# Performance work log

Measured on AMD Instinct MI355X. Metric: run time of the kernel, lower is better.

The kernel has to match this reference:

```python
import jax, jax.numpy as jnp
import numpy as np

S, B, E, H = 2048, 2, 1024, 16
HD = E // H

def setup_inputs() -> dict:
    key = jax.random.key(0)
    ks = jax.random.split(key, 5)
    return {
        "query": jax.random.normal(ks[0], (S, B, E), dtype=jnp.float32),
        "key": jax.random.normal(ks[1], (S, B, E), dtype=jnp.float32),
        "value": jax.random.normal(ks[2], (S, B, E), dtype=jnp.float32),
        "in_proj_weight": jax.random.normal(ks[3], (3 * E, E), dtype=jnp.float32) * (E ** -0.5),
        "out_weight": jax.random.normal(ks[4], (E, E), dtype=jnp.float32) * (E ** -0.5),
    }

def reference(query, key, value, in_proj_weight, out_weight):
    # query: [S, B, E]; key/value are ignored by the original self-attn module.
    seq_len, bsz, embed_dim = query.shape
    head_dim = embed_dim // H
    scaling = head_dim ** -0.5
    # qkv projection: [S, B, 3E]; the torch view splits 3E as (H, 3, head_dim)
    qkv = jnp.einsum('sbe,fe->sbf', query, in_proj_weight)
    qkv = qkv.reshape(seq_len, bsz, H, 3, head_dim)
    q = qkv[..., 0, :]  # [S, B, H, hd]
    k = qkv[..., 1, :]
    v = qkv[..., 2, :]
    # scores: [B, H, S, S] (materialized, as in the unfused original)
    scores = jnp.einsum('sbhd,tbhd->bhst', q, k) * scaling
    probs = jax.nn.softmax(scores, axis=-1)
    attn = jnp.einsum('bhst,tbhd->sbhd', probs, v)
    attn = attn.reshape(seq_len, bsz, embed_dim)
    out = jnp.einsum('sbe,fe->sbf', attn, out_weight)
    return out
```

## Files before the change

### kernel.cpp

```cpp
#include <hip/hip_runtime.h>

typedef __attribute__((ext_vector_type(8))) short bf16x8;
typedef __attribute__((ext_vector_type(4))) float f32x4;
typedef __attribute__((ext_vector_type(8))) unsigned short u16x8;
typedef __attribute__((ext_vector_type(4))) unsigned short u16x4;

#define S_LEN 2048
#define BATCH 2
#define EMB 1024
#define NH 16
#define HDIM 64
#define M_ROWS (S_LEN * BATCH)
#define N_QKV (3 * EMB)

typedef const __attribute__((address_space(1))) unsigned int* gptr_t;
typedef __attribute__((address_space(3))) unsigned int* lptr_t;

__device__ __forceinline__ unsigned short f2b(float f) {
  union { float f; unsigned u; } v; v.f = f;
  unsigned r = v.u + 0x7fff + ((v.u >> 16) & 1);
  return (unsigned short)(r >> 16);
}
__device__ __forceinline__ unsigned short f2b_fast(float f) {
  union { float f; unsigned u; } v; v.f = f;
  return (unsigned short)((v.u + 0x8000u) >> 16);
}
__device__ __forceinline__ float b2f(unsigned short s) {
  union { float f; unsigned u; } v; v.u = ((unsigned)s) << 16;
  return v.f;
}

__global__ __launch_bounds__(256) void cvt_f32_bf16(const float* __restrict__ in,
                                                    unsigned short* __restrict__ out,
                                                    int n4) {
  int i = blockIdx.x * 256 + threadIdx.x;
  if (i >= n4) return;
  float4 a = reinterpret_cast<const float4*>(in)[i];
  u16x4 o;
  o[0] = f2b(a.x); o[1] = f2b(a.y); o[2] = f2b(a.z); o[3] = f2b(a.w);
  reinterpret_cast<u16x4*>(out)[i] = o;
}

template <int OUT_BF16>
__global__ __launch_bounds__(256) void gemm_bt(const unsigned short* __restrict__ A,
                                               const unsigned short* __restrict__ Bm,
                                               void* __restrict__ Cv,
                                               int Md, int Nd, int Kd) {
  __shared__ unsigned short As[128][32];
  __shared__ unsigned short Bs[128][32];
  int t = threadIdx.x;
  int bm = blockIdx.y, bn = blockIdx.x;
  int wid = t >> 6, lane = t & 63;
  int wr = wid >> 1, wc = wid & 1;
  int fr = lane & 15, fq = lane >> 4;
  int lrow = lane >> 2;
  int lcol = (lane & 3) * 8;

  f32x4 acc[4][4];
#pragma unroll
  for (int i = 0; i < 4; ++i)
#pragma unroll
    for (int j = 0; j < 4; ++j) acc[i][j] = (f32x4){0.f, 0.f, 0.f, 0.f};

  int nkt = Kd >> 5;
  for (int kt = 0; kt < nkt; ++kt) {
    const unsigned short* ga = A + (size_t)(bm * 128 + wid * 32 + lrow) * Kd + kt * 32 + lcol;
    const unsigned short* gb = Bm + (size_t)(bn * 128 + wid * 32 + lrow) * Kd + kt * 32 + lcol;
#pragma unroll
    for (int j = 0; j < 2; ++j) {
      __builtin_amdgcn_global_load_lds((gptr_t)(ga + (size_t)j * 16 * Kd),
                                       (lptr_t)&As[wid * 32 + j * 16][0], 16, 0, 0);
      __builtin_amdgcn_global_load_lds((gptr_t)(gb + (size_t)j * 16 * Kd),
                                       (lptr_t)&Bs[wid * 32 + j * 16][0], 16, 0, 0);
    }
    __syncthreads();

    bf16x8 af[4], bfv[4];
#pragma unroll
    for (int mt = 0; mt < 4; ++mt)
      af[mt] = *reinterpret_cast<const bf16x8*>(&As[wr * 64 + mt * 16 + fr][fq * 8]);
#pragma unroll
    for (int nt = 0; nt < 4; ++nt)
      bfv[nt] = *reinterpret_cast<const bf16x8*>(&Bs[wc * 64 + nt * 16 + fr][fq * 8]);
#pragma unroll
    for (int mt = 0; mt < 4; ++mt)
#pragma unroll
      for (int nt = 0; nt < 4; ++nt)
        acc[mt][nt] = __builtin_amdgcn_mfma_f32_16x16x32_bf16(af[mt], bfv[nt], acc[mt][nt], 0, 0, 0);
    __syncthreads();
  }

#pragma unroll
  for (int mt = 0; mt < 4; ++mt)
#pragma unroll
    for (int nt = 0; nt < 4; ++nt)
#pragma unroll
      for (int r = 0; r < 4; ++r) {
        int row = bm * 128 + wr * 64 + mt * 16 + fq * 4 + r;
        int col = bn * 128 + wc * 64 + nt * 16 + fr;
        float val = acc[mt][nt][r];
        if (OUT_BF16)
          reinterpret_cast<unsigned short*>(Cv)[(size_t)row * Nd + col] = f2b(val);
        else
          reinterpret_cast<float*>(Cv)[(size_t)row * Nd + col] = val;
      }
}

__global__ __launch_bounds__(256) void vtrans(const unsigned short* __restrict__ qkv,
                                              unsigned short* __restrict__ vt) {
  __shared__ unsigned short Ts[64][72];
  int t = threadIdx.x;
  int kb = blockIdx.x;
  int bh = blockIdx.y;
  int b = bh >> 4, h = bh & 15;
  int k0 = kb * 64;
#pragma unroll
  for (int i = 0; i < 2; ++i) {
    int c = t + i * 256;
    int r = c >> 3, q = c & 7;
    int chunk = q ^ ((r >> 3) & 7);
    *reinterpret_cast<u16x8*>(&Ts[r][chunk * 8]) =
        *reinterpret_cast<const u16x8*>(
            qkv + ((size_t)(k0 + r) * BATCH + b) * N_QKV + h * 192 + 128 + q * 8);
  }
  __syncthreads();
#pragma unroll
  for (int i = 0; i < 2; ++i) {
    int c = t + i * 256;
    int d = c >> 3, q = c & 7;
    u16x8 o;
#pragma unroll
    for (int j = 0; j < 8; ++j) {
      int k = q * 8 + j;
      int chunk = (d >> 3) ^ q;
      o[j] = Ts[k][chunk * 8 + (d & 7)];
    }
    *reinterpret_cast<u16x8*>(&vt[((size_t)bh * 64 + d) * S_LEN + k0 + q * 8]) = o;
  }
}

__global__ __launch_bounds__(256) void attn_kernel(const unsigned short* __restrict__ qkv,
                                                   const unsigned short* __restrict__ vt,
                                                   unsigned short* __restrict__ att) {
  __shared__ unsigned short Ks[2][64][72];
  __shared__ unsigned short VtS[2][64][72];
  __shared__ unsigned short Ps[4][16][72];
  int t = threadIdx.x;
  int wid = t >> 6, lane = t & 63;
  int fr = lane & 15, fq = lane >> 4;
  int bh = blockIdx.y;
  int b = bh >> 4;
  int h = bh & 15;
  int q0 = blockIdx.x * 64;

  int srow = t >> 3, sc8 = (t & 7) * 8;

  int qi = q0 + wid * 16 + fr;
  const unsigned short* qrow = qkv + ((size_t)qi * BATCH + b) * N_QKV + h * 192;
  bf16x8 qf[2];
  qf[0] = *reinterpret_cast<const bf16x8*>(qrow + fq * 8);
  qf[1] = *reinterpret_cast<const bf16x8*>(qrow + 32 + fq * 8);
#pragma unroll
  for (int c = 0; c < 2; ++c)
#pragma unroll
    for (int j = 0; j < 8; ++j)
      qf[c][j] = (short)f2b_fast(0.125f * b2f((unsigned short)qf[c][j]));

  f32x4 o[4];
#pragma unroll
  for (int dt = 0; dt < 4; ++dt) o[dt] = (f32x4){0.f, 0.f, 0.f, 0.f};
  float m_run[4], l_run[4];
#pragma unroll
  for (int r = 0; r < 4; ++r) { m_run[r] = -1e30f; l_run[r] = 0.f; }

#pragma unroll
  for (int i = 0; i < 2; ++i) {
    int row = srow + i * 32;
    *reinterpret_cast<u16x8*>(&Ks[0][row][sc8]) = *reinterpret_cast<const u16x8*>(
        qkv + ((size_t)row * BATCH + b) * N_QKV + h * 192 + 64 + sc8);
    *reinterpret_cast<u16x8*>(&VtS[0][row][sc8]) = *reinterpret_cast<const u16x8*>(
        vt + ((size_t)bh * 64 + row) * S_LEN + sc8);
  }
  __syncthreads();

  for (int kt = 0; kt < S_LEN / 64; ++kt) {
    int cur = kt & 1, nxt = cur ^ 1;

    u16x8 kreg[2], vreg[2];
    if (kt + 1 < S_LEN / 64) {
#pragma unroll
      for (int i = 0; i < 2; ++i) {
        int row = srow + i * 32;
        kreg[i] = *reinterpret_cast<const u16x8*>(
            qkv + ((size_t)((kt + 1) * 64 + row) * BATCH + b) * N_QKV + h * 192 + 64 + sc8);
        vreg[i] = *reinterpret_cast<const u16x8*>(
            vt + ((size_t)bh * 64 + row) * S_LEN + (kt + 1) * 64 + sc8);
      }
    }

    f32x4 sf[4];
#pragma unroll
    for (int nt = 0; nt < 4; ++nt) {
      bf16x8 bk0 = *reinterpret_cast<const bf16x8*>(&Ks[cur][nt * 16 + fr][fq * 8]);
      bf16x8 bk1 = *reinterpret_cast<const bf16x8*>(&Ks[cur][nt * 16 + fr][32 + fq * 8]);
      f32x4 s = (f32x4){0.f, 0.f, 0.f, 0.f};
      s = __builtin_amdgcn_mfma_f32_16x16x32_bf16(qf[0], bk0, s, 0, 0, 0);
      s = __builtin_amdgcn_mfma_f32_16x16x32_bf16(qf[1], bk1, s, 0, 0, 0);
      sf[nt] = s;
    }

    float p[4][4];
#pragma unroll
    for (int r = 0; r < 4; ++r) {
      float mx = fmaxf(fmaxf(sf[0][r], sf[1][r]), fmaxf(sf[2][r], sf[3][r]));
#pragma unroll
      for (int m = 1; m < 16; m <<= 1) mx = fmaxf(mx, __shfl_xor(mx, m));
      float mnew = fmaxf(m_run[r], mx);
      float alpha = __expf(m_run[r] - mnew);
      m_run[r] = mnew;
      float rs = 0.f;
#pragma unroll
      for (int nt = 0; nt < 4; ++nt) {
        float pv = __expf(sf[nt][r] - mnew);
        p[nt][r] = pv;
        rs += pv;
      }
#pragma unroll
      for (int m = 1; m < 16; m <<= 1) rs += __shfl_xor(rs, m);
      l_run[r] = l_run[r] * alpha + rs;
#pragma unroll
      for (int dt = 0; dt < 4; ++dt) o[dt][r] *= alpha;
    }

#pragma unroll
    for (int nt = 0; nt < 4; ++nt)
#pragma unroll
      for (int r = 0; r < 4; ++r)
        Ps[wid][fq * 4 + r][nt * 16 + fr] = f2b_fast(p[nt][r]);

#pragma unroll
    for (int kc = 0; kc < 2; ++kc) {
      bf16x8 pa = *reinterpret_cast<const bf16x8*>(&Ps[wid][fr][kc * 32 + fq * 8]);
#pragma unroll
      for (int dt = 0; dt < 4; ++dt) {
        bf16x8 vb = *reinterpret_cast<const bf16x8*>(&VtS[cur][dt * 16 + fr][kc * 32 + fq * 8]);
        o[dt] = __builtin_amdgcn_mfma_f32_16x16x32_bf16(pa, vb, o[dt], 0, 0, 0);
      }
    }

    if (kt + 1 < S_LEN / 64) {
#pragma unroll
      for (int i = 0; i < 2; ++i) {
        int row = srow + i * 32;
        *reinterpret_cast<u16x8*>(&Ks[nxt][row][sc8]) = kreg[i];
        *reinterpret_cast<u16x8*>(&VtS[nxt][row][sc8]) = vreg[i];
      }
    }
    __syncthreads();
  }

#pragma unroll
  for (int dt = 0; dt < 4; ++dt)
#pragma unroll
    for (int r = 0; r < 4; ++r) {
      int q = q0 + wid * 16 + fq * 4 + r;
      int d = dt * 16 + fr;
      float val = o[dt][r] / l_run[r];
      att[((size_t)q * BATCH + b) * EMB + h * 64 + d] = f2b(val);
    }
}

extern "C" void kernel_launch(void* const* d_in, const int* in_sizes, int n_in,
                              void* d_out, int out_size, void* d_ws, size_t ws_size,
                              hipStream_t stream) {
  const float* q_in  = (const float*)d_in[0];
  const float* w_in  = (const float*)d_in[3];
  const float* w_out = (const float*)d_in[4];
  float* out = (float*)d_out;

  unsigned short* ws  = (unsigned short*)d_ws;
  unsigned short* Xb  = ws;
  unsigned short* Wb  = Xb + (size_t)M_ROWS * EMB;
  unsigned short* Ob  = Wb + (size_t)N_QKV * EMB;
  unsigned short* QKV = Ob + (size_t)EMB * EMB;
  unsigned short* ATT = QKV + (size_t)M_ROWS * N_QKV;
  unsigned short* Vt  = Xb;

  cvt_f32_bf16<<<(M_ROWS * EMB / 4 + 255) / 256, 256, 0, stream>>>(q_in, Xb, M_ROWS * EMB / 4);
  cvt_f32_bf16<<<(N_QKV * EMB / 4 + 255) / 256, 256, 0, stream>>>(w_in, Wb, N_QKV * EMB / 4);
  cvt_f32_bf16<<<(EMB * EMB / 4 + 255) / 256, 256, 0, stream>>>(w_out, Ob, EMB * EMB / 4);

  gemm_bt<1><<<dim3(N_QKV / 128, M_ROWS / 128), 256, 0, stream>>>(Xb, Wb, QKV, M_ROWS, N_QKV, EMB);
  vtrans<<<dim3(S_LEN / 64, BATCH * NH), 256, 0, stream>>>(QKV, Vt);
  attn_kernel<<<dim3(S_LEN / 64, BATCH * NH), 256, 0, stream>>>(QKV, Vt, ATT);
  gemm_bt<0><<<dim3(EMB / 128, M_ROWS / 128), 256, 0, stream>>>(ATT, Ob, out, M_ROWS, EMB, EMB);
}
```

Measured before the change: 294.9 us.

## Transpose attention MFMA operands to keep P in registers and drop LDS staging

Swaps the A/B operands of the QK^T and PV MFMAs so each lane holds scores for a single query row. The row max and sum then need only two cross-lane shuffles instead of four per row, and the softmax state collapses to one scalar per lane. The P tile is regathered into MFMA operand layout with register shuffles rather than a round trip through shared memory, which removes the Ps buffer. The output is written as 4-wide vector stores, at the cost of extra shuffle and select instructions per tile.

```diff
diff --git a/kernel.cpp b/kernel.cpp
--- a/kernel.cpp
+++ b/kernel.cpp
@@ -144,7 +144,6 @@
                                                    unsigned short* __restrict__ att) {
   __shared__ unsigned short Ks[2][64][72];
   __shared__ unsigned short VtS[2][64][72];
-  __shared__ unsigned short Ps[4][16][72];
   int t = threadIdx.x;
   int wid = t >> 6, lane = t & 63;
   int fr = lane & 15, fq = lane >> 4;
@@ -169,9 +168,11 @@
   f32x4 o[4];
 #pragma unroll
   for (int dt = 0; dt < 4; ++dt) o[dt] = (f32x4){0.f, 0.f, 0.f, 0.f};
-  float m_run[4], l_run[4];
-#pragma unroll
-  for (int r = 0; r < 4; ++r) { m_run[r] = -1e30f; l_run[r] = 0.f; }
+  float m_run = -1e30f, l_run = 0.f;
+
+  int srcA = fr + ((fq & 1) << 5);
+  int srcB = srcA + 16;
+  int hi = (fq >> 1) & 1;
 
 #pragma unroll
   for (int i = 0; i < 2; ++i) {
@@ -198,53 +199,69 @@
       }
     }
 
-    f32x4 sf[4];
+    f32x4 snt[4];
 #pragma unroll
     for (int nt = 0; nt < 4; ++nt) {
       bf16x8 bk0 = *reinterpret_cast<const bf16x8*>(&Ks[cur][nt * 16 + fr][fq * 8]);
       bf16x8 bk1 = *reinterpret_cast<const bf16x8*>(&Ks[cur][nt * 16 + fr][32 + fq * 8]);
       f32x4 s = (f32x4){0.f, 0.f, 0.f, 0.f};
-      s = __builtin_amdgcn_mfma_f32_16x16x32_bf16(qf[0], bk0, s, 0, 0, 0);
-      s = __builtin_amdgcn_mfma_f32_16x16x32_bf16(qf[1], bk1, s, 0, 0, 0);
-      sf[nt] = s;
-    }
-
-    float p[4][4];
-#pragma unroll
-    for (int r = 0; r < 4; ++r) {
-      float mx = fmaxf(fmaxf(sf[0][r], sf[1][r]), fmaxf(sf[2][r], sf[3][r]));
-#pragma unroll
-      for (int m = 1; m < 16; m <<= 1) mx = fmaxf(mx, __shfl_xor(mx, m));
-      float mnew = fmaxf(m_run[r], mx);
-      float alpha = __expf(m_run[r] - mnew);
-      m_run[r] = mnew;
-      float rs = 0.f;
-#pragma unroll
-      for (int nt = 0; nt < 4; ++nt) {
-        float pv = __expf(sf[nt][r] - mnew);
-        p[nt][r] = pv;
+      s = __builtin_amdgcn_mfma_f32_16x16x32_bf16(bk0, qf[0], s, 0, 0, 0);
+      s = __builtin_amdgcn_mfma_f32_16x16x32_bf16(bk1, qf[1], s, 0, 0, 0);
+      snt[nt] = s;
+    }
+
+    float mx = fmaxf(fmaxf(fmaxf(snt[0][0], snt[0][1]), fmaxf(snt[0][2], snt[0][3])),
+                     fmaxf(fmaxf(snt[1][0], snt[1][1]), fmaxf(snt[1][2], snt[1][3])));
+    mx = fmaxf(mx, fmaxf(fmaxf(fmaxf(snt[2][0], snt[2][1]), fmaxf(snt[2][2], snt[2][3])),
+                         fmaxf(fmaxf(snt[3][0], snt[3][1]), fmaxf(snt[3][2], snt[3][3]))));
+    mx = fmaxf(mx, __shfl_xor(mx, 16));
+    mx = fmaxf(mx, __shfl_xor(mx, 32));
+    float mnew = fmaxf(m_run, mx);
+    float alpha = __expf(m_run - mnew);
+    m_run = mnew;
+    float rs = 0.f;
+#pragma unroll
+    for (int nt = 0; nt < 4; ++nt)
+#pragma unroll
+      for (int r = 0; r < 4; ++r) {
+        float pv = __expf(snt[nt][r] - mnew);
+        snt[nt][r] = pv;
         rs += pv;
       }
-#pragma unroll
-      for (int m = 1; m < 16; m <<= 1) rs += __shfl_xor(rs, m);
-      l_run[r] = l_run[r] * alpha + rs;
-#pragma unroll
-      for (int dt = 0; dt < 4; ++dt) o[dt][r] *= alpha;
-    }
-
+    rs += __shfl_xor(rs, 16);
+    rs += __shfl_xor(rs, 32);
+    l_run = l_run * alpha + rs;
+#pragma unroll
+    for (int dt = 0; dt < 4; ++dt) o[dt] *= alpha;
+
+    unsigned pd[8];
 #pragma unroll
     for (int nt = 0; nt < 4; ++nt)
 #pragma unroll
-      for (int r = 0; r < 4; ++r)
-        Ps[wid][fq * 4 + r][nt * 16 + fr] = f2b_fast(p[nt][r]);
+      for (int hh = 0; hh < 2; ++hh)
+        pd[nt * 2 + hh] = (unsigned)f2b_fast(snt[nt][2 * hh]) |
+                          ((unsigned)f2b_fast(snt[nt][2 * hh + 1]) << 16);
 
 #pragma unroll
     for (int kc = 0; kc < 2; ++kc) {
-      bf16x8 pa = *reinterpret_cast<const bf16x8*>(&Ps[wid][fr][kc * 32 + fq * 8]);
+      int base = kc * 4;
+      unsigned a0 = (unsigned)__shfl((int)pd[base + 0], srcA);
+      unsigned a1 = (unsigned)__shfl((int)pd[base + 1], srcA);
+      unsigned a2 = (unsigned)__shfl((int)pd[base + 2], srcA);
+      unsigned a3 = (unsigned)__shfl((int)pd[base + 3], srcA);
+      unsigned c0 = (unsigned)__shfl((int)pd[base + 0], srcB);
+      unsigned c1 = (unsigned)__shfl((int)pd[base + 1], srcB);
+      unsigned c2 = (unsigned)__shfl((int)pd[base + 2], srcB);
+      unsigned c3 = (unsigned)__shfl((int)pd[base + 3], srcB);
+      union { unsigned u[4]; bf16x8 v; } pb;
+      pb.u[0] = hi ? a2 : a0;
+      pb.u[1] = hi ? a3 : a1;
+      pb.u[2] = hi ? c2 : c0;
+      pb.u[3] = hi ? c3 : c1;
 #pragma unroll
       for (int dt = 0; dt < 4; ++dt) {
         bf16x8 vb = *reinterpret_cast<const bf16x8*>(&VtS[cur][dt * 16 + fr][kc * 32 + fq * 8]);
-        o[dt] = __builtin_amdgcn_mfma_f32_16x16x32_bf16(pa, vb, o[dt], 0, 0, 0);
+        o[dt] = __builtin_amdgcn_mfma_f32_16x16x32_bf16(vb, pb.v, o[dt], 0, 0, 0);
       }
     }
 
@@ -259,15 +276,16 @@
     __syncthreads();
   }
 
-#pragma unroll
-  for (int dt = 0; dt < 4; ++dt)
-#pragma unroll
-    for (int r = 0; r < 4; ++r) {
-      int q = q0 + wid * 16 + fq * 4 + r;
-      int d = dt * 16 + fr;
-      float val = o[dt][r] / l_run[r];
-      att[((size_t)q * BATCH + b) * EMB + h * 64 + d] = f2b(val);
-    }
+  float invl = 1.0f / l_run;
+  int q = q0 + wid * 16 + fr;
+#pragma unroll
+  for (int dt = 0; dt < 4; ++dt) {
+    u16x4 ov;
+#pragma unroll
+    for (int r = 0; r < 4; ++r) ov[r] = f2b(o[dt][r] * invl);
+    int d = dt * 16 + fq * 4;
+    *reinterpret_cast<u16x4*>(&att[((size_t)q * BATCH + b) * EMB + h * 64 + d]) = ov;
+  }
 }
 
 extern "C" void kernel_launch(void* const* d_in, const int* in_sizes, int n_in,
```

Measured after the change: 253.7 us. -14.0%, faster.

## Restructure attention to 128-query blocks with transposed MFMA and lazy rescale

Applied to the files above, without the earlier changes.

The attention kernel now handles two 16-query tiles per wave (128 queries per block), so each K/V tile loaded into LDS is reused twice. It computes S^T via swapped MFMA operands so each lane owns a query column, which reduces the softmax reductions to two cross-lane shuffles. P is passed to the PV MFMA through register shuffles instead of an LDS round trip, and the output rescale is skipped unless the row max grows by more than 8. The QKV/out GEMMs also load a 64-wide K slab per barrier pair, halving synchronisations at the cost of doubled LDS; the grid for attention halves, which may reduce occupancy.

```diff
diff --git a/kernel.cpp b/kernel.cpp
--- a/kernel.cpp
+++ b/kernel.cpp
@@ -46,8 +46,8 @@
                                                const unsigned short* __restrict__ Bm,
                                                void* __restrict__ Cv,
                                                int Md, int Nd, int Kd) {
-  __shared__ unsigned short As[128][32];
-  __shared__ unsigned short Bs[128][32];
+  __shared__ unsigned short As[2][128][32];
+  __shared__ unsigned short Bs[2][128][32];
   int t = threadIdx.x;
   int bm = blockIdx.y, bn = blockIdx.x;
   int wid = t >> 6, lane = t & 63;
@@ -62,31 +62,39 @@
 #pragma unroll
     for (int j = 0; j < 4; ++j) acc[i][j] = (f32x4){0.f, 0.f, 0.f, 0.f};
 
-  int nkt = Kd >> 5;
+  int nkt = Kd >> 6;
   for (int kt = 0; kt < nkt; ++kt) {
-    const unsigned short* ga = A + (size_t)(bm * 128 + wid * 32 + lrow) * Kd + kt * 32 + lcol;
-    const unsigned short* gb = Bm + (size_t)(bn * 128 + wid * 32 + lrow) * Kd + kt * 32 + lcol;
-#pragma unroll
-    for (int j = 0; j < 2; ++j) {
-      __builtin_amdgcn_global_load_lds((gptr_t)(ga + (size_t)j * 16 * Kd),
-                                       (lptr_t)&As[wid * 32 + j * 16][0], 16, 0, 0);
-      __builtin_amdgcn_global_load_lds((gptr_t)(gb + (size_t)j * 16 * Kd),
-                                       (lptr_t)&Bs[wid * 32 + j * 16][0], 16, 0, 0);
+#pragma unroll
+    for (int hf = 0; hf < 2; ++hf) {
+      const unsigned short* ga =
+          A + (size_t)(bm * 128 + wid * 32 + lrow) * Kd + kt * 64 + hf * 32 + lcol;
+      const unsigned short* gb =
+          Bm + (size_t)(bn * 128 + wid * 32 + lrow) * Kd + kt * 64 + hf * 32 + lcol;
+#pragma unroll
+      for (int j = 0; j < 2; ++j) {
+        __builtin_amdgcn_global_load_lds((gptr_t)(ga + (size_t)j * 16 * Kd),
+                                         (lptr_t)&As[hf][wid * 32 + j * 16][0], 16, 0, 0);
+        __builtin_amdgcn_global_load_lds((gptr_t)(gb + (size_t)j * 16 * Kd),
+                                         (lptr_t)&Bs[hf][wid * 32 + j * 16][0], 16, 0, 0);
+      }
     }
     __syncthreads();
 
-    bf16x8 af[4], bfv[4];
-#pragma unroll
-    for (int mt = 0; mt < 4; ++mt)
-      af[mt] = *reinterpret_cast<const bf16x8*>(&As[wr * 64 + mt * 16 + fr][fq * 8]);
-#pragma unroll
-    for (int nt = 0; nt < 4; ++nt)
-      bfv[nt] = *reinterpret_cast<const bf16x8*>(&Bs[wc * 64 + nt * 16 + fr][fq * 8]);
-#pragma unroll
-    for (int mt = 0; mt < 4; ++mt)
+#pragma unroll
+    for (int hf = 0; hf < 2; ++hf) {
+      bf16x8 af[4], bfv[4];
+#pragma unroll
+      for (int mt = 0; mt < 4; ++mt)
+        af[mt] = *reinterpret_cast<const bf16x8*>(&As[hf][wr * 64 + mt * 16 + fr][fq * 8]);
 #pragma unroll
       for (int nt = 0; nt < 4; ++nt)
-        acc[mt][nt] = __builtin_amdgcn_mfma_f32_16x16x32_bf16(af[mt], bfv[nt], acc[mt][nt], 0, 0, 0);
+        bfv[nt] = *reinterpret_cast<const bf16x8*>(&Bs[hf][wc * 64 + nt * 16 + fr][fq * 8]);
+#pragma unroll
+      for (int mt = 0; mt < 4; ++mt)
+#pragma unroll
+        for (int nt = 0; nt < 4; ++nt)
+          acc[mt][nt] = __builtin_amdgcn_mfma_f32_16x16x32_bf16(af[mt], bfv[nt], acc[mt][nt], 0, 0, 0);
+    }
     __syncthreads();
   }
 
@@ -144,34 +152,42 @@
                                                    unsigned short* __restrict__ att) {
   __shared__ unsigned short Ks[2][64][72];
   __shared__ unsigned short VtS[2][64][72];
-  __shared__ unsigned short Ps[4][16][72];
   int t = threadIdx.x;
   int wid = t >> 6, lane = t & 63;
   int fr = lane & 15, fq = lane >> 4;
   int bh = blockIdx.y;
   int b = bh >> 4;
   int h = bh & 15;
-  int q0 = blockIdx.x * 64;
+  int q0 = blockIdx.x * 128;
 
   int srow = t >> 3, sc8 = (t & 7) * 8;
 
-  int qi = q0 + wid * 16 + fr;
-  const unsigned short* qrow = qkv + ((size_t)qi * BATCH + b) * N_QKV + h * 192;
-  bf16x8 qf[2];
-  qf[0] = *reinterpret_cast<const bf16x8*>(qrow + fq * 8);
-  qf[1] = *reinterpret_cast<const bf16x8*>(qrow + 32 + fq * 8);
-#pragma unroll
-  for (int c = 0; c < 2; ++c)
-#pragma unroll
-    for (int j = 0; j < 8; ++j)
-      qf[c][j] = (short)f2b_fast(0.125f * b2f((unsigned short)qf[c][j]));
-
-  f32x4 o[4];
-#pragma unroll
-  for (int dt = 0; dt < 4; ++dt) o[dt] = (f32x4){0.f, 0.f, 0.f, 0.f};
-  float m_run[4], l_run[4];
-#pragma unroll
-  for (int r = 0; r < 4; ++r) { m_run[r] = -1e30f; l_run[r] = 0.f; }
+  int qiA = q0 + wid * 16 + fr;
+  const unsigned short* qrowA = qkv + ((size_t)qiA * BATCH + b) * N_QKV + h * 192;
+  const unsigned short* qrowB = qrowA + (size_t)64 * BATCH * N_QKV;
+  bf16x8 qfA0 = *reinterpret_cast<const bf16x8*>(qrowA + fq * 8);
+  bf16x8 qfA1 = *reinterpret_cast<const bf16x8*>(qrowA + 32 + fq * 8);
+  bf16x8 qfB0 = *reinterpret_cast<const bf16x8*>(qrowB + fq * 8);
+  bf16x8 qfB1 = *reinterpret_cast<const bf16x8*>(qrowB + 32 + fq * 8);
+#pragma unroll
+  for (int j = 0; j < 8; ++j) {
+    qfA0[j] = (short)f2b_fast(0.125f * b2f((unsigned short)qfA0[j]));
+    qfA1[j] = (short)f2b_fast(0.125f * b2f((unsigned short)qfA1[j]));
+    qfB0[j] = (short)f2b_fast(0.125f * b2f((unsigned short)qfB0[j]));
+    qfB1[j] = (short)f2b_fast(0.125f * b2f((unsigned short)qfB1[j]));
+  }
+
+  f32x4 oA[4], oB[4];
+#pragma unroll
+  for (int dt = 0; dt < 4; ++dt) {
+    oA[dt] = (f32x4){0.f, 0.f, 0.f, 0.f};
+    oB[dt] = (f32x4){0.f, 0.f, 0.f, 0.f};
+  }
+  float mA = -1e30f, lA = 0.f, mB = -1e30f, lB = 0.f;
+
+  int sl0 = fr + ((fq & 1) << 5);
+  int sl1 = sl0 + 16;
+  int hi = (fq >> 1) & 1;
 
 #pragma unroll
   for (int i = 0; i < 2; ++i) {
@@ -198,53 +214,113 @@
       }
     }
 
-    f32x4 sf[4];
+    f32x4 sA[4], sB[4];
 #pragma unroll
     for (int nt = 0; nt < 4; ++nt) {
       bf16x8 bk0 = *reinterpret_cast<const bf16x8*>(&Ks[cur][nt * 16 + fr][fq * 8]);
       bf16x8 bk1 = *reinterpret_cast<const bf16x8*>(&Ks[cur][nt * 16 + fr][32 + fq * 8]);
-      f32x4 s = (f32x4){0.f, 0.f, 0.f, 0.f};
-      s = __builtin_amdgcn_mfma_f32_16x16x32_bf16(qf[0], bk0, s, 0, 0, 0);
-      s = __builtin_amdgcn_mfma_f32_16x16x32_bf16(qf[1], bk1, s, 0, 0, 0);
-      sf[nt] = s;
-    }
-
-    float p[4][4];
-#pragma unroll
-    for (int r = 0; r < 4; ++r) {
-      float mx = fmaxf(fmaxf(sf[0][r], sf[1][r]), fmaxf(sf[2][r], sf[3][r]));
-#pragma unroll
-      for (int m = 1; m < 16; m <<= 1) mx = fmaxf(mx, __shfl_xor(mx, m));
-      float mnew = fmaxf(m_run[r], mx);
-      float alpha = __expf(m_run[r] - mnew);
-      m_run[r] = mnew;
-      float rs = 0.f;
-#pragma unroll
-      for (int nt = 0; nt < 4; ++nt) {
-        float pv = __expf(sf[nt][r] - mnew);
-        p[nt][r] = pv;
-        rs += pv;
-      }
-#pragma unroll
-      for (int m = 1; m < 16; m <<= 1) rs += __shfl_xor(rs, m);
-      l_run[r] = l_run[r] * alpha + rs;
-#pragma unroll
-      for (int dt = 0; dt < 4; ++dt) o[dt][r] *= alpha;
-    }
-
+      f32x4 x = (f32x4){0.f, 0.f, 0.f, 0.f};
+      x = __builtin_amdgcn_mfma_f32_16x16x32_bf16(bk0, qfA0, x, 0, 0, 0);
+      x = __builtin_amdgcn_mfma_f32_16x16x32_bf16(bk1, qfA1, x, 0, 0, 0);
+      sA[nt] = x;
+      f32x4 y = (f32x4){0.f, 0.f, 0.f, 0.f};
+      y = __builtin_amdgcn_mfma_f32_16x16x32_bf16(bk0, qfB0, y, 0, 0, 0);
+      y = __builtin_amdgcn_mfma_f32_16x16x32_bf16(bk1, qfB1, y, 0, 0, 0);
+      sB[nt] = y;
+    }
+
+    float ma = fmaxf(fmaxf(sA[0][0], sA[0][1]), sA[0][2]);
+    ma = fmaxf(fmaxf(ma, sA[0][3]), sA[1][0]);
+    ma = fmaxf(fmaxf(ma, sA[1][1]), sA[1][2]);
+    float mc = fmaxf(fmaxf(sA[2][0], sA[2][1]), sA[2][2]);
+    mc = fmaxf(fmaxf(mc, sA[2][3]), sA[3][0]);
+    mc = fmaxf(fmaxf(mc, sA[3][1]), sA[3][2]);
+    float mxA = fmaxf(fmaxf(ma, sA[1][3]), fmaxf(mc, sA[3][3]));
+    mxA = fmaxf(mxA, __shfl_xor(mxA, 16));
+    mxA = fmaxf(mxA, __shfl_xor(mxA, 32));
+    float mb = fmaxf(fmaxf(sB[0][0], sB[0][1]), sB[0][2]);
+    mb = fmaxf(fmaxf(mb, sB[0][3]), sB[1][0]);
+    mb = fmaxf(fmaxf(mb, sB[1][1]), sB[1][2]);
+    float md = fmaxf(fmaxf(sB[2][0], sB[2][1]), sB[2][2]);
+    md = fmaxf(fmaxf(md, sB[2][3]), sB[3][0]);
+    md = fmaxf(fmaxf(md, sB[3][1]), sB[3][2]);
+    float mxB = fmaxf(fmaxf(mb, sB[1][3]), fmaxf(md, sB[3][3]));
+    mxB = fmaxf(mxB, __shfl_xor(mxB, 16));
+    mxB = fmaxf(mxB, __shfl_xor(mxB, 32));
+
+    if (!__all(mxA - mA <= 8.0f)) {
+      float mnew = fmaxf(mA, mxA);
+      float alpha = __expf(mA - mnew);
+      mA = mnew; lA *= alpha;
+#pragma unroll
+      for (int dt = 0; dt < 4; ++dt) oA[dt] *= alpha;
+    }
+    if (!__all(mxB - mB <= 8.0f)) {
+      float mnew = fmaxf(mB, mxB);
+      float alpha = __expf(mB - mnew);
+      mB = mnew; lB *= alpha;
+#pragma unroll
+      for (int dt = 0; dt < 4; ++dt) oB[dt] *= alpha;
+    }
+
+    float rsA = 0.f, rsB = 0.f;
 #pragma unroll
     for (int nt = 0; nt < 4; ++nt)
 #pragma unroll
-      for (int r = 0; r < 4; ++r)
-        Ps[wid][fq * 4 + r][nt * 16 + fr] = f2b_fast(p[nt][r]);
+      for (int r = 0; r < 4; ++r) {
+        float pa = __expf(sA[nt][r] - mA);
+        sA[nt][r] = pa; rsA += pa;
+        float pb = __expf(sB[nt][r] - mB);
+        sB[nt][r] = pb; rsB += pb;
+      }
+    rsA += __shfl_xor(rsA, 16); rsA += __shfl_xor(rsA, 32); lA += rsA;
+    rsB += __shfl_xor(rsB, 16); rsB += __shfl_xor(rsB, 32); lB += rsB;
+
+    unsigned pdA[8], pdB[8];
+#pragma unroll
+    for (int nt = 0; nt < 4; ++nt)
+#pragma unroll
+      for (int hh = 0; hh < 2; ++hh) {
+        asm("v_cvt_pk_bf16_f32 %0, %1, %2"
+            : "=v"(pdA[nt * 2 + hh]) : "v"(sA[nt][2 * hh]), "v"(sA[nt][2 * hh + 1]));
+        asm("v_cvt_pk_bf16_f32 %0, %1, %2"
+            : "=v"(pdB[nt * 2 + hh]) : "v"(sB[nt][2 * hh]), "v"(sB[nt][2 * hh + 1]));
+      }
 
 #pragma unroll
     for (int kc = 0; kc < 2; ++kc) {
-      bf16x8 pa = *reinterpret_cast<const bf16x8*>(&Ps[wid][fr][kc * 32 + fq * 8]);
+      int base = kc * 4;
+      unsigned aA0 = (unsigned)__shfl((int)pdA[base + 0], sl0);
+      unsigned aA1 = (unsigned)__shfl((int)pdA[base + 1], sl0);
+      unsigned aA2 = (unsigned)__shfl((int)pdA[base + 2], sl0);
+      unsigned aA3 = (unsigned)__shfl((int)pdA[base + 3], sl0);
+      unsigned cA0 = (unsigned)__shfl((int)pdA[base + 0], sl1);
+      unsigned cA1 = (unsigned)__shfl((int)pdA[base + 1], sl1);
+      unsigned cA2 = (unsigned)__shfl((int)pdA[base + 2], sl1);
+      unsigned cA3 = (unsigned)__shfl((int)pdA[base + 3], sl1);
+      union { unsigned u[4]; bf16x8 v; } pbA;
+      pbA.u[0] = hi ? aA2 : aA0;
+      pbA.u[1] = hi ? aA3 : aA1;
+      pbA.u[2] = hi ? cA2 : cA0;
+      pbA.u[3] = hi ? cA3 : cA1;
+      unsigned aB0 = (unsigned)__shfl((int)pdB[base + 0], sl0);
+      unsigned aB1 = (unsigned)__shfl((int)pdB[base + 1], sl0);
+      unsigned aB2 = (unsigned)__shfl((int)pdB[base + 2], sl0);
+      unsigned aB3 = (unsigned)__shfl((int)pdB[base + 3], sl0);
+      unsigned cB0 = (unsigned)__shfl((int)pdB[base + 0], sl1);
+      unsigned cB1 = (unsigned)__shfl((int)pdB[base + 1], sl1);
+      unsigned cB2 = (unsigned)__shfl((int)pdB[base + 2], sl1);
+      unsigned cB3 = (unsigned)__shfl((int)pdB[base + 3], sl1);
+      union { unsigned u[4]; bf16x8 v; } pbB;
+      pbB.u[0] = hi ? aB2 : aB0;
+      pbB.u[1] = hi ? aB3 : aB1;
+      pbB.u[2] = hi ? cB2 : cB0;
+      pbB.u[3] = hi ? cB3 : cB1;
 #pragma unroll
       for (int dt = 0; dt < 4; ++dt) {
         bf16x8 vb = *reinterpret_cast<const bf16x8*>(&VtS[cur][dt * 16 + fr][kc * 32 + fq * 8]);
-        o[dt] = __builtin_amdgcn_mfma_f32_16x16x32_bf16(pa, vb, o[dt], 0, 0, 0);
+        oA[dt] = __builtin_amdgcn_mfma_f32_16x16x32_bf16(vb, pbA.v, oA[dt], 0, 0, 0);
+        oB[dt] = __builtin_amdgcn_mfma_f32_16x16x32_bf16(vb, pbB.v, oB[dt], 0, 0, 0);
       }
     }
 
@@ -259,15 +335,20 @@
     __syncthreads();
   }
 
-#pragma unroll
-  for (int dt = 0; dt < 4; ++dt)
+  float invlA = 1.0f / lA, invlB = 1.0f / lB;
+  int qA = q0 + wid * 16 + fr;
+#pragma unroll
+  for (int dt = 0; dt < 4; ++dt) {
+    u16x4 ovA, ovB;
 #pragma unroll
     for (int r = 0; r < 4; ++r) {
-      int q = q0 + wid * 16 + fq * 4 + r;
-      int d = dt * 16 + fr;
-      float val = o[dt][r] / l_run[r];
-      att[((size_t)q * BATCH + b) * EMB + h * 64 + d] = f2b(val);
-    }
+      ovA[r] = f2b(oA[dt][r] * invlA);
+      ovB[r] = f2b(oB[dt][r] * invlB);
+    }
+    int d = dt * 16 + fq * 4;
+    *reinterpret_cast<u16x4*>(&att[((size_t)qA * BATCH + b) * EMB + h * 64 + d]) = ovA;
+    *reinterpret_cast<u16x4*>(&att[((size_t)(qA + 64) * BATCH + b) * EMB + h * 64 + d]) = ovB;
+  }
 }
 
 extern "C" void kernel_launch(void* const* d_in, const int* in_sizes, int n_in,
@@ -292,6 +373,6 @@
 
   gemm_bt<1><<<dim3(N_QKV / 128, M_ROWS / 128), 256, 0, stream>>>(Xb, Wb, QKV, M_ROWS, N_QKV, EMB);
   vtrans<<<dim3(S_LEN / 64, BATCH * NH), 256, 0, stream>>>(QKV, Vt);
-  attn_kernel<<<dim3(S_LEN / 64, BATCH * NH), 256, 0, stream>>>(QKV, Vt, ATT);
+  attn_kernel<<<dim3(S_LEN / 128, BATCH * NH), 256, 0, stream>>>(QKV, Vt, ATT);
   gemm_bt<0><<<dim3(EMB / 128, M_ROWS / 128), 256, 0, stream>>>(ATT, Ob, out, M_ROWS, EMB, EMB);
 }
```

Measured after the change: 238.0 us. 19.3% less time.
